# Optimization experiments

Measured on AMD Instinct MI355X. Metric: run time of the kernel, lower is better.

The kernel has to match this reference:

```python
import jax, jax.numpy as jnp
import numpy as np

N = 131072      # total nodes in batch
D = 128         # input_dim
K_EXP = 1024    # input_dim * num_conv_kernels
H = 512         # cluster_model_hidden_dim
NG = 4          # number of groups (sub-models)
F_SEG = 8192    # fine clusters (global_max_pool segments)
G_SEG = 32      # coarse graphs (InstanceNorm segments)
C = 16          # node_num_classes
EPS = 1e-5      # InstanceNorm eps


def setup_inputs() -> dict:
    key = jax.random.key(0)
    ks = jax.random.split(key, 8)
    x = jax.random.normal(ks[0], (N, D), jnp.float32)
    # disjoint partition of node indices into NG groups (gather/scatter dispatch)
    group_indices = jax.random.permutation(ks[1], N).reshape(NG, N // NG)
    # sorted segment ids, every segment non-empty
    pool_cluster_fine = (jnp.arange(N) // (N // F_SEG)).astype(jnp.int32)
    batch_cluster_coarse = (jnp.arange(F_SEG) // (F_SEG // G_SEG)).astype(jnp.int32)
    # per-group NodeModel params: expand D -> K_EXP, relu, project -> H
    W1 = jax.random.normal(ks[2], (NG, D, K_EXP), jnp.float32) * (1.0 / np.sqrt(D))
    b1 = jnp.zeros((NG, K_EXP), jnp.float32)
    W2 = jax.random.normal(ks[3], (NG, K_EXP, H), jnp.float32) * (1.0 / np.sqrt(K_EXP))
    b2 = jnp.zeros((NG, H), jnp.float32)
    # classifier (glorot weight, zero bias)
    w_out = jax.random.normal(ks[4], (H, C), jnp.float32) * np.sqrt(2.0 / (H + C))
    b_out = jnp.zeros((C,), jnp.float32)
    return {"x": x, "group_indices": group_indices,
            "pool_cluster_fine": pool_cluster_fine,
            "batch_cluster_coarse": batch_cluster_coarse,
            "W1": W1, "b1": b1, "W2": W2, "b2": b2,
            "w_out": w_out, "b_out": b_out}


def reference(x, group_indices, pool_cluster_fine, batch_cluster_coarse,
              W1, b1, W2, b2, w_out, b_out):
    # per-group gather -> sub-model -> scatter (vectorized over groups)
    xg = x[group_indices]                                   # [NG, N/NG, D]
    h = jax.nn.relu(jnp.einsum('gnd,gdk->gnk', xg, W1) + b1[:, None, :])
    og = jnp.einsum('gnk,gkh->gnh', h, W2) + b2[:, None, :]  # [NG, N/NG, H]
    new_feat = jnp.zeros((x.shape[0], H), x.dtype).at[group_indices.reshape(-1)].set(
        og.reshape(-1, H))                                   # [N, H]
    # global_max_pool over fine clusters
    emb = jax.ops.segment_max(new_feat, pool_cluster_fine,
                              num_segments=F_SEG, indices_are_sorted=True)  # [F, H]
    # PyG InstanceNorm(affine=False): per coarse-graph, per-channel standardization
    ones = jnp.ones((F_SEG, 1), emb.dtype)
    cnt = jax.ops.segment_sum(ones, batch_cluster_coarse,
                              num_segments=G_SEG, indices_are_sorted=True)  # [G,1]
    mean = jax.ops.segment_sum(emb, batch_cluster_coarse,
                               num_segments=G_SEG, indices_are_sorted=True) / cnt
    var = jax.ops.segment_sum(emb * emb, batch_cluster_coarse,
                              num_segments=G_SEG, indices_are_sorted=True) / cnt - mean ** 2
    normed = (emb - mean[batch_cluster_coarse]) * jax.lax.rsqrt(var[batch_cluster_coarse] + EPS)
    # dropout is identity in eval mode; classifier
    logits = normed @ w_out + b_out                          # [F, C]
    return logits
```

## Files before the change

kernel.cpp:

```cpp
#include <hip/hip_runtime.h>
#include <stdint.h>

typedef __bf16 bf16;
typedef bf16 bf16x4 __attribute__((ext_vector_type(4)));
typedef bf16 bf16x8 __attribute__((ext_vector_type(8)));
typedef float f32x4 __attribute__((ext_vector_type(4)));

#define N_NODES 131072
#define D_IN    128
#define KEXP    1024
#define H_DIM   512
#define NGRP    4
#define NPG     32768
#define F_SEG   8192
#define G_SEG   32
#define C_OUT   16

typedef const __attribute__((address_space(1))) void* gas_t;
typedef __attribute__((address_space(3))) void* las_t;
__device__ __forceinline__ void cp16_async(const bf16* g, bf16* l) {
    __builtin_amdgcn_global_load_lds((gas_t)g, (las_t)l, 16, 0, 0);
}

__global__ void convert_weights(const float* __restrict__ W1,
                                const float* __restrict__ W2,
                                bf16* __restrict__ W1F,
                                bf16* __restrict__ W2F)
{
    int t = blockIdx.x * 256 + threadIdx.x;
    if (t < 65536) {
        int slot = t & 63, f = (t >> 6) & 7, kc = (t >> 9) & 31, g = t >> 14;
        int ks = f >> 1, kt = f & 1, quad = slot >> 4, ln = slot & 15;
        int k = kc * 32 + kt * 16 + ln;
        const float* src = W1 + ((size_t)(g * 128 + ks * 32 + quad * 8)) * 1024 + k;
        bf16x8 v;
        #pragma unroll
        for (int j = 0; j < 8; ++j) v[j] = (bf16)src[(size_t)j * 1024];
        *(bf16x8*)(W1F + (size_t)t * 8) = v;
    } else {
        int u = t - 65536;
        if (u < 262144) {
            int slot = u & 63, f = (u >> 6) & 15, kc = (u >> 10) & 31;
            int n0t2 = (u >> 15) & 1, g = u >> 16;
            int quad = slot >> 4, ln = slot & 15;
            int k = kc * 32 + quad * 8;
            int n = n0t2 * 256 + f * 16 + ln;
            const float* src = W2 + ((size_t)(g * 1024 + k)) * 512 + n;
            bf16x8 v;
            #pragma unroll
            for (int j = 0; j < 8; ++j) v[j] = (bf16)src[(size_t)j * 512];
            *(bf16x8*)(W2F + (size_t)u * 8) = v;
        }
    }
}

__global__ __launch_bounds__(256, 2)
void mlp_kernel(const float* __restrict__ x,
                const int*   __restrict__ gidx,
                const bf16*  __restrict__ W1F,
                const float* __restrict__ b1,
                const bf16*  __restrict__ W2F,
                const float* __restrict__ b2,
                bf16*        __restrict__ NF)
{
    __shared__ __align__(16) bf16 sW1[2][4096];
    __shared__ __align__(16) bf16 sH[2][2048];
    __shared__ __align__(16) float sB1[1024];

    const int tid  = threadIdx.x;
    const int bid  = blockIdx.x;
    const int g    = bid >> 9;
    const int m0   = (bid & 511) * 64;

    const int wave = tid >> 6;
    const int lane = tid & 63;
    const int quad = lane >> 4;
    const int ln   = lane & 15;

    const int*  gI  = gidx + g * NPG + m0;
    const bf16* W1g = W1F + (size_t)g * 131072;
    const bf16* W2g2 = W2F + ((size_t)(g * 2 + (wave >> 1))) * 262144
                     + (wave & 1) * 4096;

    bf16x8 xf[4];
    #pragma unroll
    for (int ks = 0; ks < 4; ++ks) {
        int node = gI[wave * 16 + ln];
        const float* src = x + (size_t)node * D_IN + ks * 32 + quad * 8;
        float4 a = *(const float4*)src;
        float4 b = *(const float4*)(src + 4);
        bf16x8 v;
        v[0] = (bf16)a.x; v[1] = (bf16)a.y; v[2] = (bf16)a.z; v[3] = (bf16)a.w;
        v[4] = (bf16)b.x; v[5] = (bf16)b.y; v[6] = (bf16)b.z; v[7] = (bf16)b.w;
        xf[ks] = v;
    }

    *(float4*)(sB1 + tid * 4) = *(const float4*)(b1 + g * KEXP + tid * 4);

    f32x4 acc2[4][8];
    #pragma unroll
    for (int a = 0; a < 4; ++a)
        #pragma unroll
        for (int b = 0; b < 8; ++b)
            acc2[a][b] = (f32x4){0.f, 0.f, 0.f, 0.f};

    auto do_stage1 = [&](int j) {
        const bf16* w1buf = sW1[j & 1];
        bf16*       hdst  = sH[j & 1];
        f32x4 acc1[2];
        acc1[0] = (f32x4){0.f, 0.f, 0.f, 0.f};
        acc1[1] = (f32x4){0.f, 0.f, 0.f, 0.f};
        #pragma unroll
        for (int ks = 0; ks < 4; ++ks) {
            #pragma unroll
            for (int kt = 0; kt < 2; ++kt) {
                bf16x8 w1f = *(const bf16x8*)(w1buf + ((ks * 2 + kt) * 64 + lane) * 8);
                acc1[kt] = __builtin_amdgcn_mfma_f32_16x16x32_bf16(
                    w1f, xf[ks], acc1[kt], 0, 0, 0);
            }
        }
        #pragma unroll
        for (int kt = 0; kt < 2; ++kt) {
            float4 bv = *(const float4*)(sB1 + j * 32 + kt * 16 + quad * 4);
            float bvr[4] = {bv.x, bv.y, bv.z, bv.w};
            int qa = kt * 2 + (quad >> 1);
            int j0 = (quad & 1) * 4;
            bf16x4 pk;
            #pragma unroll
            for (int reg = 0; reg < 4; ++reg)
                pk[reg] = (bf16)fmaxf(acc1[kt][reg] + bvr[reg], 0.f);
            *(bf16x4*)(hdst + (wave * 64 + qa * 16 + ln) * 8 + j0) = pk;
        }
    };

    __syncthreads();

    #pragma unroll
    for (int r = 0; r < 2; ++r) {
        int c = r * 4 + wave;
        cp16_async(W1g + c * 512 + lane * 8, sW1[0] + c * 512);
    }
    #pragma unroll
    for (int r = 0; r < 2; ++r) {
        int c = r * 4 + wave;
        cp16_async(W1g + 4096 + c * 512 + lane * 8, sW1[1] + c * 512);
    }
    asm volatile("s_waitcnt vmcnt(2)" ::: "memory");
    __builtin_amdgcn_s_barrier();

    do_stage1(0);

    #pragma unroll 1
    for (int j = 1; j < 32; ++j) {
        __syncthreads();

        bf16x8 bb[8];
        {
            const bf16* w2src = W2g2 + (size_t)(j - 1) * 8192;
            #pragma unroll
            for (int nt = 0; nt < 8; ++nt)
                bb[nt] = *(const bf16x8*)(w2src + nt * 512 + lane * 8);
        }

        {
            int nkc = (j + 1) & 31;
            const bf16* w1src = W1g + (size_t)nkc * 4096;
            bf16* d1 = sW1[(j + 1) & 1];
            #pragma unroll
            for (int r = 0; r < 2; ++r) {
                int c = r * 4 + wave;
                cp16_async(w1src + c * 512 + lane * 8, d1 + c * 512);
            }
        }

        __builtin_amdgcn_s_setprio(1);
        do_stage1(j);

        {
            const bf16* hbuf = sH[(j - 1) & 1];
            #pragma unroll
            for (int mt = 0; mt < 4; ++mt) {
                bf16x8 a2 = *(const bf16x8*)(hbuf + (mt * 64 + lane) * 8);
                #pragma unroll
                for (int nt = 0; nt < 8; ++nt)
                    acc2[mt][nt] = __builtin_amdgcn_mfma_f32_16x16x32_bf16(
                        a2, bb[nt], acc2[mt][nt], 0, 0, 0);
            }
        }
        __builtin_amdgcn_s_setprio(0);
    }

    __syncthreads();
    {
        bf16x8 bb[8];
        const bf16* w2src = W2g2 + (size_t)31 * 8192;
        #pragma unroll
        for (int nt = 0; nt < 8; ++nt)
            bb[nt] = *(const bf16x8*)(w2src + nt * 512 + lane * 8);
        const bf16* hbuf = sH[1];
        #pragma unroll
        for (int mt = 0; mt < 4; ++mt) {
            bf16x8 a2 = *(const bf16x8*)(hbuf + (mt * 64 + lane) * 8);
            #pragma unroll
            for (int nt = 0; nt < 8; ++nt)
                acc2[mt][nt] = __builtin_amdgcn_mfma_f32_16x16x32_bf16(
                    a2, bb[nt], acc2[mt][nt], 0, 0, 0);
        }
    }

    const float* b2g = b2 + g * H_DIM + wave * 128;
    float b2v[8];
    #pragma unroll
    for (int nt = 0; nt < 8; ++nt) b2v[nt] = b2g[nt * 16 + ln];

    #pragma unroll
    for (int mt = 0; mt < 4; ++mt)
        #pragma unroll
        for (int reg = 0; reg < 4; ++reg) {
            int row  = mt * 16 + quad * 4 + reg;
            int node = gI[row];
            bf16* dst = NF + (size_t)node * H_DIM + wave * 128;
            #pragma unroll
            for (int nt = 0; nt < 8; ++nt)
                dst[nt * 16 + ln] = (bf16)(acc2[mt][nt][reg] + b2v[nt]);
        }
}

__global__ void pool_kernel(const bf16* __restrict__ NF, float* __restrict__ EMB)
{
    int t  = blockIdx.x * 256 + threadIdx.x;
    int f  = t >> 6;
    int c8 = (t & 63) * 8;
    const uint4* src = (const uint4*)(NF + (size_t)f * 16 * 512 + c8);
    float m[8];
    #pragma unroll
    for (int i = 0; i < 8; ++i) m[i] = -INFINITY;
    #pragma unroll
    for (int r = 0; r < 16; ++r) {
        uint4 v = src[(size_t)r * 64];
        uint32_t w[4] = {v.x, v.y, v.z, v.w};
        #pragma unroll
        for (int i = 0; i < 4; ++i) {
            m[2*i]   = fmaxf(m[2*i],   __uint_as_float(w[i] << 16));
            m[2*i+1] = fmaxf(m[2*i+1], __uint_as_float(w[i] & 0xffff0000u));
        }
    }
    float* dst = EMB + (size_t)f * 512 + c8;
    *(float4*)dst       = make_float4(m[0], m[1], m[2], m[3]);
    *(float4*)(dst + 4) = make_float4(m[4], m[5], m[6], m[7]);
}

__global__ void stats_kernel(const float* __restrict__ EMB,
                             float* __restrict__ MEAN,
                             float* __restrict__ RSIG)
{
    int gc = blockIdx.x;
    int ch = blockIdx.y * 128 + threadIdx.x;
    const float* p = EMB + (size_t)gc * 256 * 512 + ch;
    float s = 0.f, ss = 0.f;
    #pragma unroll 4
    for (int r = 0; r < 256; ++r) {
        float v = p[(size_t)r * 512];
        s += v; ss += v * v;
    }
    float mean = s * (1.f / 256.f);
    float var  = ss * (1.f / 256.f) - mean * mean;
    MEAN[gc * 512 + ch] = mean;
    RSIG[gc * 512 + ch] = rsqrtf(var + 1e-5f);
}

__global__ __launch_bounds__(256)
void classifier_kernel(const float* __restrict__ EMB,
                       const float* __restrict__ MEAN,
                       const float* __restrict__ RSIG,
                       const float* __restrict__ w_out,
                       const float* __restrict__ b_out,
                       float* __restrict__ out)
{
    __shared__ float sW[512 * 16];
    __shared__ float sE[16 * 513];
    int t  = threadIdx.x;
    int f0 = blockIdx.x * 16;
    int gc = f0 >> 8;

    #pragma unroll
    for (int it = 0; it < 8; ++it) {
        int i = (it * 256 + t) * 4;
        *(float4*)(sW + i) = *(const float4*)(w_out + i);
    }
    #pragma unroll
    for (int it = 0; it < 32; ++it) {
        int i  = it * 256 + t;
        int fr = i >> 9;
        int h  = i & 511;
        float v = EMB[(size_t)(f0 + fr) * 512 + h];
        sE[fr * 513 + h] = (v - MEAN[gc * 512 + h]) * RSIG[gc * 512 + h];
    }
    __syncthreads();

    int fr = t >> 4;
    int c  = t & 15;
    float acc = b_out[c];
    #pragma unroll 8
    for (int h = 0; h < 512; ++h)
        acc += sE[fr * 513 + h] * sW[h * 16 + c];
    out[(size_t)(f0 + fr) * 16 + c] = acc;
}

extern "C" void kernel_launch(void* const* d_in, const int* in_sizes, int n_in,
                              void* d_out, int out_size, void* d_ws, size_t ws_size,
                              hipStream_t stream)
{
    const float* x     = (const float*)d_in[0];
    const int*   gidx  = (const int*)d_in[1];
    const float* W1    = (const float*)d_in[4];
    const float* b1    = (const float*)d_in[5];
    const float* W2    = (const float*)d_in[6];
    const float* b2    = (const float*)d_in[7];
    const float* w_out = (const float*)d_in[8];
    const float* b_out = (const float*)d_in[9];
    float* out = (float*)d_out;

    char* w = (char*)d_ws;
    bf16* W1F = (bf16*)w;  w += (size_t)NGRP * KEXP * D_IN * 2;
    bf16* W2F = (bf16*)w;  w += (size_t)NGRP * H_DIM * KEXP * 2;
    bf16* NF  = (bf16*)w;  w += (size_t)N_NODES * H_DIM * 2;
    float* EMB  = (float*)w; w += (size_t)F_SEG * H_DIM * 4;
    float* MEAN = (float*)w; w += (size_t)G_SEG * H_DIM * 4;
    float* RSIG = (float*)w; w += (size_t)G_SEG * H_DIM * 4;

    convert_weights<<<1280, 256, 0, stream>>>(W1, W2, W1F, W2F);
    mlp_kernel<<<2048, 256, 0, stream>>>(x, gidx, W1F, b1, W2F, b2, NF);
    pool_kernel<<<2048, 256, 0, stream>>>(NF, EMB);
    stats_kernel<<<dim3(32, 4), 128, 0, stream>>>(EMB, MEAN, RSIG);
    classifier_kernel<<<512, 256, 0, stream>>>(EMB, MEAN, RSIG, w_out, b_out, out);
}
```

Before: 341.1 us.

## Split MLP block work across eight waves with half-width per-wave tiles

The fused MLP kernel moves from 4 waves to 8 waves per block. Each wave now computes one 16-row stage-1 tile and a 64-column slice of the second GEMM instead of 128 columns. This halves per-wave accumulator registers and aims at higher occupancy (launch bounds 512,4) and more latency hiding. The cost is duplicated x loads per wave pair, more waves contending at each barrier, and a shared-memory budget that may cap how many blocks are actually resident.

New measurement: 340.1 us. Within noise of the previous version (-0.3%).

```diff
diff --git a/kernel.cpp b/kernel.cpp
--- a/kernel.cpp
+++ b/kernel.cpp
@@ -54,7 +54,7 @@
     }
 }
 
-__global__ __launch_bounds__(256, 2)
+__global__ __launch_bounds__(512, 4)
 void mlp_kernel(const float* __restrict__ x,
                 const int*   __restrict__ gidx,
                 const bf16*  __restrict__ W1F,
@@ -77,75 +77,63 @@
     const int quad = lane >> 4;
     const int ln   = lane & 15;
 
+    const int rf = wave & 3;
+    const int kt = wave >> 2;
+
     const int*  gI  = gidx + g * NPG + m0;
     const bf16* W1g = W1F + (size_t)g * 131072;
-    const bf16* W2g2 = W2F + ((size_t)(g * 2 + (wave >> 1))) * 262144
-                     + (wave & 1) * 4096;
+    const bf16* W2g2 = W2F + ((size_t)(g * 2 + (wave >> 2))) * 262144
+                     + (size_t)((wave & 3) * 4) * 512;
 
     bf16x8 xf[4];
-    #pragma unroll
-    for (int ks = 0; ks < 4; ++ks) {
-        int node = gI[wave * 16 + ln];
-        const float* src = x + (size_t)node * D_IN + ks * 32 + quad * 8;
-        float4 a = *(const float4*)src;
-        float4 b = *(const float4*)(src + 4);
-        bf16x8 v;
-        v[0] = (bf16)a.x; v[1] = (bf16)a.y; v[2] = (bf16)a.z; v[3] = (bf16)a.w;
-        v[4] = (bf16)b.x; v[5] = (bf16)b.y; v[6] = (bf16)b.z; v[7] = (bf16)b.w;
-        xf[ks] = v;
-    }
-
-    *(float4*)(sB1 + tid * 4) = *(const float4*)(b1 + g * KEXP + tid * 4);
-
-    f32x4 acc2[4][8];
+    {
+        int node = gI[rf * 16 + ln];
+        #pragma unroll
+        for (int ks = 0; ks < 4; ++ks) {
+            const float* src = x + (size_t)node * D_IN + ks * 32 + quad * 8;
+            float4 a = *(const float4*)src;
+            float4 b = *(const float4*)(src + 4);
+            bf16x8 v;
+            v[0] = (bf16)a.x; v[1] = (bf16)a.y; v[2] = (bf16)a.z; v[3] = (bf16)a.w;
+            v[4] = (bf16)b.x; v[5] = (bf16)b.y; v[6] = (bf16)b.z; v[7] = (bf16)b.w;
+            xf[ks] = v;
+        }
+    }
+
+    *(float2*)(sB1 + tid * 2) = *(const float2*)(b1 + g * KEXP + tid * 2);
+
+    f32x4 acc2[4][4];
     #pragma unroll
     for (int a = 0; a < 4; ++a)
         #pragma unroll
-        for (int b = 0; b < 8; ++b)
+        for (int b = 0; b < 4; ++b)
             acc2[a][b] = (f32x4){0.f, 0.f, 0.f, 0.f};
 
     auto do_stage1 = [&](int j) {
         const bf16* w1buf = sW1[j & 1];
         bf16*       hdst  = sH[j & 1];
-        f32x4 acc1[2];
-        acc1[0] = (f32x4){0.f, 0.f, 0.f, 0.f};
-        acc1[1] = (f32x4){0.f, 0.f, 0.f, 0.f};
+        f32x4 acc1 = (f32x4){0.f, 0.f, 0.f, 0.f};
         #pragma unroll
         for (int ks = 0; ks < 4; ++ks) {
-            #pragma unroll
-            for (int kt = 0; kt < 2; ++kt) {
-                bf16x8 w1f = *(const bf16x8*)(w1buf + ((ks * 2 + kt) * 64 + lane) * 8);
-                acc1[kt] = __builtin_amdgcn_mfma_f32_16x16x32_bf16(
-                    w1f, xf[ks], acc1[kt], 0, 0, 0);
-            }
-        }
-        #pragma unroll
-        for (int kt = 0; kt < 2; ++kt) {
-            float4 bv = *(const float4*)(sB1 + j * 32 + kt * 16 + quad * 4);
-            float bvr[4] = {bv.x, bv.y, bv.z, bv.w};
-            int qa = kt * 2 + (quad >> 1);
-            int j0 = (quad & 1) * 4;
-            bf16x4 pk;
-            #pragma unroll
-            for (int reg = 0; reg < 4; ++reg)
-                pk[reg] = (bf16)fmaxf(acc1[kt][reg] + bvr[reg], 0.f);
-            *(bf16x4*)(hdst + (wave * 64 + qa * 16 + ln) * 8 + j0) = pk;
-        }
+            bf16x8 w1f = *(const bf16x8*)(w1buf + ((ks * 2 + kt) * 64 + lane) * 8);
+            acc1 = __builtin_amdgcn_mfma_f32_16x16x32_bf16(w1f, xf[ks], acc1, 0, 0, 0);
+        }
+        float4 bv = *(const float4*)(sB1 + j * 32 + kt * 16 + quad * 4);
+        float bvr[4] = {bv.x, bv.y, bv.z, bv.w};
+        int qa = kt * 2 + (quad >> 1);
+        int j0 = (quad & 1) * 4;
+        bf16x4 pk;
+        #pragma unroll
+        for (int reg = 0; reg < 4; ++reg)
+            pk[reg] = (bf16)fmaxf(acc1[reg] + bvr[reg], 0.f);
+        *(bf16x4*)(hdst + (rf * 64 + qa * 16 + ln) * 8 + j0) = pk;
     };
 
     __syncthreads();
 
-    #pragma unroll
-    for (int r = 0; r < 2; ++r) {
-        int c = r * 4 + wave;
-        cp16_async(W1g + c * 512 + lane * 8, sW1[0] + c * 512);
-    }
-    #pragma unroll
-    for (int r = 0; r < 2; ++r) {
-        int c = r * 4 + wave;
-        cp16_async(W1g + 4096 + c * 512 + lane * 8, sW1[1] + c * 512);
-    }
-    asm volatile("s_waitcnt vmcnt(2)" ::: "memory");
+    cp16_async(W1g + wave * 512 + lane * 8, sW1[0] + wave * 512);
+    cp16_async(W1g + 4096 + wave * 512 + lane * 8, sW1[1] + wave * 512);
+    asm volatile("s_waitcnt vmcnt(1)" ::: "memory");
     __builtin_amdgcn_s_barrier();
 
     do_stage1(0);
@@ -154,23 +142,18 @@
     for (int j = 1; j < 32; ++j) {
         __syncthreads();
 
-        bf16x8 bb[8];
+        bf16x8 bb[4];
         {
             const bf16* w2src = W2g2 + (size_t)(j - 1) * 8192;
             #pragma unroll
-            for (int nt = 0; nt < 8; ++nt)
-                bb[nt] = *(const bf16x8*)(w2src + nt * 512 + lane * 8);
+            for (int n = 0; n < 4; ++n)
+                bb[n] = *(const bf16x8*)(w2src + n * 512 + lane * 8);
         }
 
         {
             int nkc = (j + 1) & 31;
-            const bf16* w1src = W1g + (size_t)nkc * 4096;
-            bf16* d1 = sW1[(j + 1) & 1];
-            #pragma unroll
-            for (int r = 0; r < 2; ++r) {
-                int c = r * 4 + wave;
-                cp16_async(w1src + c * 512 + lane * 8, d1 + c * 512);
-            }
+            cp16_async(W1g + (size_t)nkc * 4096 + wave * 512 + lane * 8,
+                       sW1[(j + 1) & 1] + wave * 512);
         }
 
         __builtin_amdgcn_s_setprio(1);
@@ -182,9 +165,9 @@
             for (int mt = 0; mt < 4; ++mt) {
                 bf16x8 a2 = *(const bf16x8*)(hbuf + (mt * 64 + lane) * 8);
                 #pragma unroll
-                for (int nt = 0; nt < 8; ++nt)
-                    acc2[mt][nt] = __builtin_amdgcn_mfma_f32_16x16x32_bf16(
-                        a2, bb[nt], acc2[mt][nt], 0, 0, 0);
+                for (int n = 0; n < 4; ++n)
+                    acc2[mt][n] = __builtin_amdgcn_mfma_f32_16x16x32_bf16(
+                        a2, bb[n], acc2[mt][n], 0, 0, 0);
             }
         }
         __builtin_amdgcn_s_setprio(0);
@@ -192,26 +175,26 @@
 
     __syncthreads();
     {
-        bf16x8 bb[8];
+        bf16x8 bb[4];
         const bf16* w2src = W2g2 + (size_t)31 * 8192;
         #pragma unroll
-        for (int nt = 0; nt < 8; ++nt)
-            bb[nt] = *(const bf16x8*)(w2src + nt * 512 + lane * 8);
+        for (int n = 0; n < 4; ++n)
+            bb[n] = *(const bf16x8*)(w2src + n * 512 + lane * 8);
         const bf16* hbuf = sH[1];
         #pragma unroll
         for (int mt = 0; mt < 4; ++mt) {
             bf16x8 a2 = *(const bf16x8*)(hbuf + (mt * 64 + lane) * 8);
             #pragma unroll
-            for (int nt = 0; nt < 8; ++nt)
-                acc2[mt][nt] = __builtin_amdgcn_mfma_f32_16x16x32_bf16(
-                    a2, bb[nt], acc2[mt][nt], 0, 0, 0);
-        }
-    }
-
-    const float* b2g = b2 + g * H_DIM + wave * 128;
-    float b2v[8];
-    #pragma unroll
-    for (int nt = 0; nt < 8; ++nt) b2v[nt] = b2g[nt * 16 + ln];
+            for (int n = 0; n < 4; ++n)
+                acc2[mt][n] = __builtin_amdgcn_mfma_f32_16x16x32_bf16(
+                    a2, bb[n], acc2[mt][n], 0, 0, 0);
+        }
+    }
+
+    const float* b2g = b2 + g * H_DIM + wave * 64;
+    float b2v[4];
+    #pragma unroll
+    for (int n = 0; n < 4; ++n) b2v[n] = b2g[n * 16 + ln];
 
     #pragma unroll
     for (int mt = 0; mt < 4; ++mt)
@@ -219,10 +202,10 @@
         for (int reg = 0; reg < 4; ++reg) {
             int row  = mt * 16 + quad * 4 + reg;
             int node = gI[row];
-            bf16* dst = NF + (size_t)node * H_DIM + wave * 128;
-            #pragma unroll
-            for (int nt = 0; nt < 8; ++nt)
-                dst[nt * 16 + ln] = (bf16)(acc2[mt][nt][reg] + b2v[nt]);
+            bf16* dst = NF + (size_t)node * H_DIM + wave * 64;
+            #pragma unroll
+            for (int n = 0; n < 4; ++n)
+                dst[n * 16 + ln] = (bf16)(acc2[mt][n][reg] + b2v[n]);
         }
 }
 
@@ -330,7 +313,7 @@
     float* RSIG = (float*)w; w += (size_t)G_SEG * H_DIM * 4;
 
     convert_weights<<<1280, 256, 0, stream>>>(W1, W2, W1F, W2F);
-    mlp_kernel<<<2048, 256, 0, stream>>>(x, gidx, W1F, b1, W2F, b2, NF);
+    mlp_kernel<<<2048, 512, 0, stream>>>(x, gidx, W1F, b1, W2F, b2, NF);
     pool_kernel<<<2048, 256, 0, stream>>>(NF, EMB);
     stats_kernel<<<dim3(32, 4), 128, 0, stream>>>(EMB, MEAN, RSIG);
     classifier_kernel<<<512, 256, 0, stream>>>(EMB, MEAN, RSIG, w_out, b_out, out);
```
